# Kernel optimization log

Measured on AMD Instinct MI355X. Metric: run time of the kernel, lower is better.

Reference implementation:

```python
import jax, jax.numpy as jnp
import numpy as np

N_NODES = 100000
N_EDGES = 300000
HIDDEN = 256
N_TYPES = 8
VOCAB = 32000
N_STEPS = 5


def _gru_cell(x, h, w_ih, w_hh, b_ih, b_hh):
    # PyTorch GRUCell: gates ordered [reset, update, new]
    gi = x @ w_ih.T + b_ih                      # [N, 3H]
    gh = h @ w_hh.T + b_hh                      # [N, 3H]
    i_r, i_z, i_n = jnp.split(gi, 3, axis=-1)
    h_r, h_z, h_n = jnp.split(gh, 3, axis=-1)
    r = jax.nn.sigmoid(i_r + h_r)
    z = jax.nn.sigmoid(i_z + h_z)
    n = jnp.tanh(i_n + r * h_n)
    return (1.0 - z) * n + z * h


def _msg_op(h, edge_index, edge_type, W_msg, b_msg):
    # Gather source node states, apply per-edge-type linear, scatter-add to dst.
    src, dst = edge_index[0], edge_index[1]
    h_src = h[src]                               # [E, H]
    msgs = jnp.zeros_like(h_src)
    for t in range(N_TYPES):                     # small fixed loop over edge types
        m_t = h_src @ W_msg[t] + b_msg[t]        # [E, H]
        msgs = jnp.where((edge_type == t)[:, None], m_t, msgs)
    return jax.ops.segment_sum(msgs, dst, num_segments=h.shape[0])  # [N, H]


def setup_inputs() -> dict:
    key = jax.random.key(0)
    ks = jax.random.split(key, 10)
    x = jax.random.randint(ks[0], (N_NODES,), 0, VOCAB)
    edge_index = jax.random.randint(ks[1], (2, N_EDGES), 0, N_NODES)
    edge_type = jax.random.randint(ks[2], (N_EDGES,), 0, N_TYPES)
    s = 1.0 / np.sqrt(HIDDEN)
    emb = jax.random.normal(ks[3], (VOCAB, HIDDEN), dtype=jnp.float32)
    W_msg = jax.random.uniform(ks[4], (N_TYPES, HIDDEN, HIDDEN), minval=-s, maxval=s, dtype=jnp.float32)
    b_msg = jax.random.uniform(ks[5], (N_TYPES, HIDDEN), minval=-s, maxval=s, dtype=jnp.float32)
    w_ih = jax.random.uniform(ks[6], (3 * HIDDEN, HIDDEN), minval=-s, maxval=s, dtype=jnp.float32)
    w_hh = jax.random.uniform(ks[7], (3 * HIDDEN, HIDDEN), minval=-s, maxval=s, dtype=jnp.float32)
    b_ih = jax.random.uniform(ks[8], (3 * HIDDEN,), minval=-s, maxval=s, dtype=jnp.float32)
    b_hh = jax.random.uniform(ks[9], (3 * HIDDEN,), minval=-s, maxval=s, dtype=jnp.float32)
    return {"x": x, "edge_index": edge_index, "edge_type": edge_type,
            "emb": emb, "W_msg": W_msg, "b_msg": b_msg,
            "w_ih": w_ih, "w_hh": w_hh, "b_ih": b_ih, "b_hh": b_hh}


def reference(x, edge_index, edge_type, emb, W_msg, b_msg, w_ih, w_hh, b_ih, b_hh):
    h = emb[x]                                   # [N, H] node embedding lookup
    for _ in range(N_STEPS):
        aggr = _msg_op(h, edge_index, edge_type, W_msg, b_msg)
        h = _gru_cell(aggr, h, w_ih, w_hh, b_ih, b_hh)
    return h
```

## Files before the change

### kernel.cpp

```cpp
#include <hip/hip_runtime.h>
#include <math.h>

#define NN 100000
#define NE 300000
#define H 256
#define NT 8
#define NSTEPS 5
#define CHUNK 256
#define NB ((NE + CHUNK - 1) / CHUNK)
#define NBIN ((NN + 127) / 128)
#define MAXBIN 768
#define RS 264

typedef __attribute__((ext_vector_type(8))) short bf16x8;
typedef __attribute__((ext_vector_type(4))) float f32x4;

static __device__ __forceinline__ short f2bf(float f) {
    union { float f; unsigned u; } v; v.f = f;
    unsigned r = (v.u + 0x7FFFu + ((v.u >> 16) & 1u)) >> 16;
    return (short)r;
}
static __device__ __forceinline__ float bf2f(unsigned short s) {
    union { unsigned u; float f; } v; v.u = ((unsigned)s) << 16;
    return v.f;
}
static __device__ __forceinline__ float fexp2(float x) {
    float r; asm("v_exp_f32 %0, %1" : "=v"(r) : "v"(x)); return r;
}
static __device__ __forceinline__ float frcp(float x) {
    float r; asm("v_rcp_f32 %0, %1" : "=v"(r) : "v"(x)); return r;
}
#define LOG2E 1.442695041f

__global__ void k_embed(const int* __restrict__ x, const float* __restrict__ emb,
                        short* __restrict__ h) {
    int total = NN * 32;
    for (int idx = blockIdx.x * blockDim.x + threadIdx.x; idx < total;
         idx += gridDim.x * blockDim.x) {
        int node = idx >> 5;
        int c8 = (idx & 31) * 8;
        const float4* p = reinterpret_cast<const float4*>(
            emb + (size_t)x[node] * H + c8);
        float4 u0 = p[0], u1 = p[1];
        short t[8];
        t[0] = f2bf(u0.x); t[1] = f2bf(u0.y); t[2] = f2bf(u0.z); t[3] = f2bf(u0.w);
        t[4] = f2bf(u1.x); t[5] = f2bf(u1.y); t[6] = f2bf(u1.z); t[7] = f2bf(u1.w);
        *(bf16x8*)(h + (size_t)node * H + c8) = *(bf16x8*)t;
    }
}

__global__ void k_prep(const float* __restrict__ wih, const float* __restrict__ whh,
                       const float* __restrict__ Wm,
                       short* __restrict__ wihp, short* __restrict__ whhp,
                       short* __restrict__ Wmp) {
    const int NW = 3 * H * H;
    const int NM = NT * H * H;
    for (int i = blockIdx.x * blockDim.x + threadIdx.x; i < 2 * NW + NM;
         i += gridDim.x * blockDim.x) {
        if (i < 2 * NW) {
            int which = (i >= NW);
            int j = which ? i - NW : i;
            int m = j & 7, lane = (j >> 3) & 63;
            int cc = (j >> 9) & 15, kk = (j >> 13) & 7, gate = j >> 16;
            int row = gate * H + cc * 16 + (lane & 15);
            int col = kk * 32 + (lane >> 4) * 8 + m;
            const float* src = which ? whh : wih;
            (which ? whhp : wihp)[j] = f2bf(src[(size_t)row * H + col]);
        } else {
            int j = i - 2 * NW;
            int m = j & 7, lane = (j >> 3) & 63;
            int cc = (j >> 9) & 15, kk = (j >> 13) & 7, t = j >> 16;
            int jcol = cc * 16 + (lane & 15);
            int krow = kk * 32 + (lane >> 4) * 8 + m;
            Wmp[j] = f2bf(Wm[(size_t)t * H * H + (size_t)krow * H + jcol]);
        }
    }
}

__global__ void k_hist(const int* __restrict__ etype, int* __restrict__ hist_tb) {
    __shared__ int lh[NT];
    int b = blockIdx.x;
    if (threadIdx.x < NT) lh[threadIdx.x] = 0;
    __syncthreads();
    int e = b * CHUNK + threadIdx.x;
    if (e < NE) atomicAdd(&lh[etype[e]], 1);
    __syncthreads();
    if (threadIdx.x < NT) hist_tb[threadIdx.x * NB + b] = lh[threadIdx.x];
}

__global__ void k_scan(const int* __restrict__ hist_tb, int* __restrict__ off_tb,
                       int* __restrict__ pstart, int* __restrict__ perm) {
    __shared__ int total[NT];
    int t = threadIdx.x;
    if (t < NT) {
        int run = 0;
        for (int b = 0; b < NB; b++) {
            off_tb[t * NB + b] = run;
            run += hist_tb[t * NB + b];
        }
        total[t] = run;
    }
    __syncthreads();
    if (t == 0) {
        int p = 0;
        for (int tt = 0; tt < NT; tt++) {
            pstart[tt] = p;
            int padded = (total[tt] + 127) / 128 * 128;
            for (int q = total[tt]; q < padded; q++) perm[p + q] = -1;
            p += padded;
        }
        pstart[NT] = p;
    }
}

__global__ void k_scatter(const int* __restrict__ etype, const int* __restrict__ off_tb,
                          const int* __restrict__ pstart, int* __restrict__ perm) {
    __shared__ int st[CHUNK];
    int b = blockIdx.x;
    int e = b * CHUNK + threadIdx.x;
    st[threadIdx.x] = (e < NE) ? etype[e] : -1;
    __syncthreads();
    if (e < NE) {
        int t = st[threadIdx.x];
        int r = 0;
        for (int i = 0; i < threadIdx.x; i++) r += (st[i] == t);
        perm[pstart[t] + off_tb[t * NB + b] + r] = e;
    }
}

__global__ void k_hist2(const int* __restrict__ ei, int* __restrict__ hist2) {
    __shared__ int lh[NBIN];
    int b = blockIdx.x;
    for (int i = threadIdx.x; i < NBIN; i += 256) lh[i] = 0;
    __syncthreads();
    int e = b * CHUNK + threadIdx.x;
    if (e < NE) atomicAdd(&lh[ei[NE + e] >> 7], 1);
    __syncthreads();
    for (int i = threadIdx.x; i < NBIN; i += 256) hist2[i * NB + b] = lh[i];
}

__global__ void k_scan2a(const int* __restrict__ hist2, int* __restrict__ off2,
                         int* __restrict__ bintot) {
    int t = blockIdx.x * 256 + threadIdx.x;
    if (t >= NBIN) return;
    int run = 0;
    for (int c = 0; c < NB; c++) {
        off2[t * NB + c] = run;
        run += hist2[t * NB + c];
    }
    bintot[t] = run;
}

__global__ void k_scan2b(const int* __restrict__ bintot, int* __restrict__ binstart,
                         int* __restrict__ csr) {
    int p = 0;
    for (int b = 0; b < NBIN; b++) { binstart[b] = p; p += bintot[b]; }
    binstart[NBIN] = p;
    csr[NN] = NE;
}

__global__ void k_scatter2(const int* __restrict__ ei, const int* __restrict__ off2,
                           const int* __restrict__ binstart, int* __restrict__ ebin) {
    __shared__ short sb[CHUNK];
    int b = blockIdx.x;
    int e = b * CHUNK + threadIdx.x;
    int bin = (e < NE) ? (ei[NE + e] >> 7) : -1;
    sb[threadIdx.x] = (short)bin;
    __syncthreads();
    if (e < NE) {
        int r = 0;
        for (int i = 0; i < threadIdx.x; i++) r += (sb[i] == (short)bin);
        ebin[binstart[bin] + off2[bin * NB + b] + r] = e;
    }
}

__global__ __launch_bounds__(256) void k_lsort(
    const int* __restrict__ ei, const int* __restrict__ binstart,
    const int* __restrict__ ebin, int* __restrict__ csr, int* __restrict__ pos) {
    int b = blockIdx.x;
    int beg = binstart[b], cnt = binstart[b + 1] - beg;
    __shared__ unsigned short ld[MAXBIN];
    __shared__ int lh[128], ls[128];
    for (int i = threadIdx.x; i < 128; i += 256) lh[i] = 0;
    __syncthreads();
    for (int i = threadIdx.x; i < cnt; i += 256) {
        int d = ei[NE + ebin[beg + i]] & 127;
        ld[i] = (unsigned short)d;
        atomicAdd(&lh[d], 1);
    }
    __syncthreads();
    if (threadIdx.x == 0) {
        int run = 0;
        for (int l = 0; l < 128; l++) { ls[l] = run; run += lh[l]; }
    }
    __syncthreads();
    int base = b * 128;
    for (int l = threadIdx.x; l < 128; l += 256) {
        int dst = base + l;
        if (dst < NN) csr[dst] = beg + ls[l];
    }
    for (int i = threadIdx.x; i < cnt; i += 256) {
        int d = ld[i], r = 0;
        for (int j = 0; j < i; j++) r += (ld[j] == d);
        pos[ebin[beg + i]] = beg + ls[d] + r;
    }
}

__global__ __launch_bounds__(512) void k_msg(
    const int* __restrict__ perm, const int* __restrict__ pstart,
    const int* __restrict__ ei, const short* __restrict__ hcurb,
    const short* __restrict__ Wmp, const float* __restrict__ bm,
    const int* __restrict__ pos, short* __restrict__ msg) {
    int Epad = pstart[NT];
    int e0 = blockIdx.x * 128;
    if (e0 >= Epad) return;
    int t = 0;
    while (t < NT - 1 && e0 >= pstart[t + 1]) t++;

    __shared__ short sA[128][RS];
    __shared__ int se[128], pe[128];

    int tid = threadIdx.x;
    if (tid < 128) {
        int eid = perm[e0 + tid];
        se[tid] = (eid >= 0) ? ei[eid] : -1;
        pe[tid] = (eid >= 0) ? pos[eid] : -1;
    }
    __syncthreads();

    for (int task = tid; task < 1024; task += 512) {
        int r = task >> 3, c0 = (task & 7) * 32;
        int s = se[r];
        if (s >= 0) {
            const short* p = hcurb + (size_t)s * H + c0;
#pragma unroll
            for (int i = 0; i < 4; i++)
                *(bf16x8*)&sA[r][c0 + i * 8] = *(const bf16x8*)(p + i * 8);
        } else {
            bf16x8 z = {};
#pragma unroll
            for (int i = 0; i < 4; i++) *(bf16x8*)&sA[r][c0 + i * 8] = z;
        }
    }
    __syncthreads();

    int wid = tid >> 6, lane = tid & 63;
    int jw = wid * 32;
    int lr = lane & 15, lg = lane >> 4;

    f32x4 acc[8][2] = {};

    for (int kk = 0; kk < 8; kk++) {
        const short* fp = Wmp + (((size_t)(t * 8 + kk) * 16 + wid * 2) << 9) + lane * 8;
        bf16x8 fb[2];
        fb[0] = *(const bf16x8*)fp;
        fb[1] = *(const bf16x8*)(fp + 512);
        int k0 = kk * 32;
#pragma unroll
        for (int rh = 0; rh < 8; rh++) {
            bf16x8 fa = *(const bf16x8*)&sA[rh * 16 + lr][k0 + lg * 8];
#pragma unroll
            for (int ch = 0; ch < 2; ch++)
                acc[rh][ch] = __builtin_amdgcn_mfma_f32_16x16x32_bf16(
                    fa, fb[ch], acc[rh][ch], 0, 0, 0);
        }
    }

    __syncthreads();
    float bmv[2];
#pragma unroll
    for (int ch = 0; ch < 2; ch++) bmv[ch] = bm[t * H + jw + ch * 16 + lr];
#pragma unroll
    for (int rh = 0; rh < 8; rh++) {
#pragma unroll
        for (int reg = 0; reg < 4; reg++) {
            int row = rh * 16 + lg * 4 + reg;
#pragma unroll
            for (int ch = 0; ch < 2; ch++)
                sA[row][jw + ch * 16 + lr] = f2bf(acc[rh][ch][reg] + bmv[ch]);
        }
    }
    __syncthreads();
    for (int task = tid; task < 1024; task += 512) {
        int r = task >> 3, c0 = (task & 7) * 32;
        int p = pe[r];
        if (p < 0) continue;
        short* dstp = msg + (size_t)p * H + c0;
#pragma unroll
        for (int i = 0; i < 4; i++)
            *(bf16x8*)(dstp + i * 8) = *(bf16x8*)&sA[r][c0 + i * 8];
    }
}

__global__ __launch_bounds__(512)
__attribute__((amdgpu_waves_per_eu(2))) void k_gru(
    const short* __restrict__ msg, const int* __restrict__ csr,
    const short* __restrict__ hcurb, short* __restrict__ hnextb,
    float* __restrict__ outf,
    const short* __restrict__ wihp, const short* __restrict__ whhp,
    const float* __restrict__ bih, const float* __restrict__ bhh) {
    int n0 = blockIdx.x * 64;
    int tid = threadIdx.x;

    __shared__ short sA[64][RS];
    __shared__ short sH[64][RS];

    for (int task = tid; task < 1024; task += 512) {
        int which = task >> 9;
        int t2 = task & 511;
        int r = t2 >> 3, c0 = (t2 & 7) * 32;
        int n = n0 + r;
        if (which == 0) {
            float a[32];
#pragma unroll
            for (int i = 0; i < 32; i++) a[i] = 0.f;
            if (n < NN) {
                int beg = csr[n], end = csr[n + 1];
                for (int s = beg; s < end; s++) {
                    const short* mp = msg + (size_t)s * H + c0;
#pragma unroll
                    for (int i = 0; i < 4; i++) {
                        bf16x8 v = *(const bf16x8*)(mp + i * 8);
#pragma unroll
                        for (int m = 0; m < 8; m++)
                            a[i * 8 + m] += bf2f((unsigned short)v[m]);
                    }
                }
            }
            short tmp[32];
#pragma unroll
            for (int i = 0; i < 32; i++) tmp[i] = f2bf(a[i]);
#pragma unroll
            for (int i = 0; i < 4; i++)
                *(bf16x8*)&sA[r][c0 + i * 8] = *(bf16x8*)&tmp[i * 8];
        } else {
            if (n < NN) {
                const short* p = hcurb + (size_t)n * H + c0;
#pragma unroll
                for (int i = 0; i < 4; i++)
                    *(bf16x8*)&sH[r][c0 + i * 8] = *(const bf16x8*)(p + i * 8);
            } else {
                bf16x8 z = {};
#pragma unroll
                for (int i = 0; i < 4; i++) *(bf16x8*)&sH[r][c0 + i * 8] = z;
            }
        }
    }
    __syncthreads();

    int wid = tid >> 6, lane = tid & 63;
    int jw = wid * 32;
    int lr = lane & 15, lg = lane >> 4;

    f32x4 acc[4][4][2] = {};

    for (int kk = 0; kk < 8; kk++) {
        int k0 = kk * 32;
        bf16x8 fa[4], fh[4];
#pragma unroll
        for (int rh = 0; rh < 4; rh++) {
            fa[rh] = *(const bf16x8*)&sA[rh * 16 + lr][k0 + lg * 8];
            fh[rh] = *(const bf16x8*)&sH[rh * 16 + lr][k0 + lg * 8];
        }
#pragma unroll
        for (int g = 0; g < 6; g++) {
            const short* wp = (g & 1) ? whhp : wihp;
            int gate = g >> 1;
            int di = (g < 4) ? (g >> 1) : (g - 2);
            const short* fp = wp + (((size_t)(gate * 8 + kk) * 16 + wid * 2) << 9) + lane * 8;
            bf16x8 fb[2];
            fb[0] = *(const bf16x8*)fp;
            fb[1] = *(const bf16x8*)(fp + 512);
#pragma unroll
            for (int rh = 0; rh < 4; rh++)
#pragma unroll
                for (int ch = 0; ch < 2; ch++)
                    acc[di][rh][ch] = __builtin_amdgcn_mfma_f32_16x16x32_bf16(
                        (g & 1) ? fh[rh] : fa[rh], fb[ch], acc[di][rh][ch], 0, 0, 0);
        }
    }

    float b_r[2], b_z[2], b_in[2], b_hn[2];
#pragma unroll
    for (int ch = 0; ch < 2; ch++) {
        int jj = jw + ch * 16 + lr;
        b_r[ch]  = bih[jj] + bhh[jj];
        b_z[ch]  = bih[H + jj] + bhh[H + jj];
        b_in[ch] = bih[2 * H + jj];
        b_hn[ch] = bhh[2 * H + jj];
    }
#pragma unroll
    for (int rh = 0; rh < 4; rh++) {
#pragma unroll
        for (int reg = 0; reg < 4; reg++) {
            int row = rh * 16 + lg * 4 + reg;
            int n = n0 + row;
            if (n >= NN) continue;
#pragma unroll
            for (int ch = 0; ch < 2; ch++) {
                int jj = jw + ch * 16 + lr;
                float rr = acc[0][rh][ch][reg] + b_r[ch];
                float zz = acc[1][rh][ch][reg] + b_z[ch];
                float nn = acc[2][rh][ch][reg] + b_in[ch];
                float hn = acc[3][rh][ch][reg] + b_hn[ch];
                float r = frcp(1.f + fexp2(rr * -LOG2E));
                float z = frcp(1.f + fexp2(zz * -LOG2E));
                float x = nn + r * hn;
                float nv = 2.f * frcp(1.f + fexp2(x * -2.f * LOG2E)) - 1.f;
                float ho = bf2f((unsigned short)sH[row][jj]);
                float val = (1.f - z) * nv + z * ho;
                if (outf) outf[(size_t)n * H + jj] = val;
                else hnextb[(size_t)n * H + jj] = f2bf(val);
            }
        }
    }
}

extern "C" void kernel_launch(void* const* d_in, const int* in_sizes, int n_in,
                              void* d_out, int out_size, void* d_ws, size_t ws_size,
                              hipStream_t stream) {
    const int*   x     = (const int*)d_in[0];
    const int*   ei    = (const int*)d_in[1];
    const int*   etype = (const int*)d_in[2];
    const float* emb   = (const float*)d_in[3];
    const float* Wm    = (const float*)d_in[4];
    const float* bm    = (const float*)d_in[5];
    const float* wih   = (const float*)d_in[6];
    const float* whh   = (const float*)d_in[7];
    const float* bih   = (const float*)d_in[8];
    const float* bhh   = (const float*)d_in[9];

    float* out = (float*)d_out;

    short* hA    = (short*)d_ws;
    short* hB    = hA + (size_t)NN * H;
    short* wihp  = hB + (size_t)NN * H;
    short* whhp  = wihp + 3 * H * H;
    short* Wmp   = whhp + 3 * H * H;
    short* msg   = Wmp + NT * H * H;
    int* hist_tb = (int*)(msg + (size_t)NE * H);
    int* off_tb  = hist_tb + NT * NB;
    int* pstart  = off_tb + NT * NB;
    int* perm    = pstart + 16;
    int* hist2   = perm + NE + NT * 128;
    int* off2    = hist2 + NBIN * NB;
    int* bintot  = off2 + NBIN * NB;
    int* binstart= bintot + NBIN;
    int* ebin    = binstart + NBIN + 1;
    int* pos     = ebin + NE;
    int* csr     = pos + NE;

    k_embed<<<2048, 256, 0, stream>>>(x, emb, hA);
    k_prep<<<720, 256, 0, stream>>>(wih, whh, Wm, wihp, whhp, Wmp);

    k_hist<<<NB, CHUNK, 0, stream>>>(etype, hist_tb);
    k_scan<<<1, 64, 0, stream>>>(hist_tb, off_tb, pstart, perm);
    k_scatter<<<NB, CHUNK, 0, stream>>>(etype, off_tb, pstart, perm);

    k_hist2<<<NB, CHUNK, 0, stream>>>(ei, hist2);
    k_scan2a<<<(NBIN + 255) / 256, 256, 0, stream>>>(hist2, off2, bintot);
    k_scan2b<<<1, 1, 0, stream>>>(bintot, binstart, csr);
    k_scatter2<<<NB, CHUNK, 0, stream>>>(ei, off2, binstart, ebin);
    k_lsort<<<NBIN, 256, 0, stream>>>(ei, binstart, ebin, csr, pos);

    const int MSG_BX = (NE + NT * 128 + 127) / 128;
    const int GRU_BX = (NN + 63) / 64;

    short* hcur = hA;
    short* hnxt = hB;
    for (int s = 0; s < NSTEPS; s++) {
        int last = (s == NSTEPS - 1);
        k_msg<<<MSG_BX, 512, 0, stream>>>(perm, pstart, ei, hcur, Wmp, bm, pos, msg);
        k_gru<<<GRU_BX, 512, 0, stream>>>(msg, csr, hcur, hnxt,
                                          last ? out : nullptr,
                                          wihp, whhp, bih, bhh);
        short* tmp = hcur; hcur = hnxt; hnxt = tmp;
    }
}
```

Measured before the change: 1.635 ms.

## Halve msg tile to 64 edges, single-buffer GRU LDS, coalesce hidden-state stores

```diff
diff --git a/kernel.cpp b/kernel.cpp
--- a/kernel.cpp
+++ b/kernel.cpp
@@ -105,7 +105,7 @@
         int p = 0;
         for (int tt = 0; tt < NT; tt++) {
             pstart[tt] = p;
-            int padded = (total[tt] + 127) / 128 * 128;
+            int padded = (total[tt] + 63) / 64 * 64;
             for (int q = total[tt]; q < padded; q++) perm[p + q] = -1;
             p += padded;
         }
@@ -212,24 +212,24 @@
     const short* __restrict__ Wmp, const float* __restrict__ bm,
     const int* __restrict__ pos, short* __restrict__ msg) {
     int Epad = pstart[NT];
-    int e0 = blockIdx.x * 128;
+    int e0 = blockIdx.x * 64;
     if (e0 >= Epad) return;
     int t = 0;
     while (t < NT - 1 && e0 >= pstart[t + 1]) t++;
 
-    __shared__ short sA[128][RS];
-    __shared__ int se[128], pe[128];
+    __shared__ short sA[64][RS];
+    __shared__ int se[64], pe[64];
 
     int tid = threadIdx.x;
-    if (tid < 128) {
+    if (tid < 64) {
         int eid = perm[e0 + tid];
         se[tid] = (eid >= 0) ? ei[eid] : -1;
         pe[tid] = (eid >= 0) ? pos[eid] : -1;
     }
     __syncthreads();
 
-    for (int task = tid; task < 1024; task += 512) {
-        int r = task >> 3, c0 = (task & 7) * 32;
+    {
+        int r = tid >> 3, c0 = (tid & 7) * 32;
         int s = se[r];
         if (s >= 0) {
             const short* p = hcurb + (size_t)s * H + c0;
@@ -248,7 +248,7 @@
     int jw = wid * 32;
     int lr = lane & 15, lg = lane >> 4;
 
-    f32x4 acc[8][2] = {};
+    f32x4 acc[4][2] = {};
 
     for (int kk = 0; kk < 8; kk++) {
         const short* fp = Wmp + (((size_t)(t * 8 + kk) * 16 + wid * 2) << 9) + lane * 8;
@@ -257,7 +257,7 @@
         fb[1] = *(const bf16x8*)(fp + 512);
         int k0 = kk * 32;
 #pragma unroll
-        for (int rh = 0; rh < 8; rh++) {
+        for (int rh = 0; rh < 4; rh++) {
             bf16x8 fa = *(const bf16x8*)&sA[rh * 16 + lr][k0 + lg * 8];
 #pragma unroll
             for (int ch = 0; ch < 2; ch++)
@@ -271,7 +271,7 @@
 #pragma unroll
     for (int ch = 0; ch < 2; ch++) bmv[ch] = bm[t * H + jw + ch * 16 + lr];
 #pragma unroll
-    for (int rh = 0; rh < 8; rh++) {
+    for (int rh = 0; rh < 4; rh++) {
 #pragma unroll
         for (int reg = 0; reg < 4; reg++) {
             int row = rh * 16 + lg * 4 + reg;
@@ -281,14 +281,15 @@
         }
     }
     __syncthreads();
-    for (int task = tid; task < 1024; task += 512) {
-        int r = task >> 3, c0 = (task & 7) * 32;
+    {
+        int r = tid >> 3, c0 = (tid & 7) * 32;
         int p = pe[r];
-        if (p < 0) continue;
-        short* dstp = msg + (size_t)p * H + c0;
-#pragma unroll
-        for (int i = 0; i < 4; i++)
-            *(bf16x8*)(dstp + i * 8) = *(bf16x8*)&sA[r][c0 + i * 8];
+        if (p >= 0) {
+            short* dstp = msg + (size_t)p * H + c0;
+#pragma unroll
+            for (int i = 0; i < 4; i++)
+                *(bf16x8*)(dstp + i * 8) = *(bf16x8*)&sA[r][c0 + i * 8];
+        }
     }
 }
 
@@ -302,72 +303,52 @@
     int n0 = blockIdx.x * 64;
     int tid = threadIdx.x;
 
-    __shared__ short sA[64][RS];
-    __shared__ short sH[64][RS];
-
-    for (int task = tid; task < 1024; task += 512) {
-        int which = task >> 9;
-        int t2 = task & 511;
-        int r = t2 >> 3, c0 = (t2 & 7) * 32;
-        int n = n0 + r;
-        if (which == 0) {
-            float a[32];
-#pragma unroll
-            for (int i = 0; i < 32; i++) a[i] = 0.f;
-            if (n < NN) {
-                int beg = csr[n], end = csr[n + 1];
-                for (int s = beg; s < end; s++) {
-                    const short* mp = msg + (size_t)s * H + c0;
-#pragma unroll
-                    for (int i = 0; i < 4; i++) {
-                        bf16x8 v = *(const bf16x8*)(mp + i * 8);
-#pragma unroll
-                        for (int m = 0; m < 8; m++)
-                            a[i * 8 + m] += bf2f((unsigned short)v[m]);
-                    }
-                }
-            }
-            short tmp[32];
-#pragma unroll
-            for (int i = 0; i < 32; i++) tmp[i] = f2bf(a[i]);
-#pragma unroll
-            for (int i = 0; i < 4; i++)
-                *(bf16x8*)&sA[r][c0 + i * 8] = *(bf16x8*)&tmp[i * 8];
-        } else {
-            if (n < NN) {
-                const short* p = hcurb + (size_t)n * H + c0;
-#pragma unroll
-                for (int i = 0; i < 4; i++)
-                    *(bf16x8*)&sH[r][c0 + i * 8] = *(const bf16x8*)(p + i * 8);
-            } else {
-                bf16x8 z = {};
-#pragma unroll
-                for (int i = 0; i < 4; i++) *(bf16x8*)&sH[r][c0 + i * 8] = z;
-            }
-        }
-    }
-    __syncthreads();
+    __shared__ short sX[64][RS];
 
     int wid = tid >> 6, lane = tid & 63;
     int jw = wid * 32;
     int lr = lane & 15, lg = lane >> 4;
 
+    {
+        int r = tid >> 3, c0 = (tid & 7) * 32;
+        int n = n0 + r;
+        float a[32];
+#pragma unroll
+        for (int i = 0; i < 32; i++) a[i] = 0.f;
+        if (n < NN) {
+            int beg = csr[n], end = csr[n + 1];
+            for (int s = beg; s < end; s++) {
+                const short* mp = msg + (size_t)s * H + c0;
+#pragma unroll
+                for (int i = 0; i < 4; i++) {
+                    bf16x8 v = *(const bf16x8*)(mp + i * 8);
+#pragma unroll
+                    for (int m = 0; m < 8; m++)
+                        a[i * 8 + m] += bf2f((unsigned short)v[m]);
+                }
+            }
+        }
+        short tmp[32];
+#pragma unroll
+        for (int i = 0; i < 32; i++) tmp[i] = f2bf(a[i]);
+#pragma unroll
+        for (int i = 0; i < 4; i++)
+            *(bf16x8*)&sX[r][c0 + i * 8] = *(bf16x8*)&tmp[i * 8];
+    }
+    __syncthreads();
+
     f32x4 acc[4][4][2] = {};
 
     for (int kk = 0; kk < 8; kk++) {
         int k0 = kk * 32;
-        bf16x8 fa[4], fh[4];
-#pragma unroll
-        for (int rh = 0; rh < 4; rh++) {
-            fa[rh] = *(const bf16x8*)&sA[rh * 16 + lr][k0 + lg * 8];
-            fh[rh] = *(const bf16x8*)&sH[rh * 16 + lr][k0 + lg * 8];
-        }
-#pragma unroll
-        for (int g = 0; g < 6; g++) {
-            const short* wp = (g & 1) ? whhp : wihp;
-            int gate = g >> 1;
-            int di = (g < 4) ? (g >> 1) : (g - 2);
-            const short* fp = wp + (((size_t)(gate * 8 + kk) * 16 + wid * 2) << 9) + lane * 8;
+        bf16x8 fa[4];
+#pragma unroll
+        for (int rh = 0; rh < 4; rh++)
+            fa[rh] = *(const bf16x8*)&sX[rh * 16 + lr][k0 + lg * 8];
+#pragma unroll
+        for (int gate = 0; gate < 3; gate++) {
+            int di = (gate < 2) ? gate : 2;
+            const short* fp = wihp + (((size_t)(gate * 8 + kk) * 16 + wid * 2) << 9) + lane * 8;
             bf16x8 fb[2];
             fb[0] = *(const bf16x8*)fp;
             fb[1] = *(const bf16x8*)(fp + 512);
@@ -376,7 +357,46 @@
 #pragma unroll
                 for (int ch = 0; ch < 2; ch++)
                     acc[di][rh][ch] = __builtin_amdgcn_mfma_f32_16x16x32_bf16(
-                        (g & 1) ? fh[rh] : fa[rh], fb[ch], acc[di][rh][ch], 0, 0, 0);
+                        fa[rh], fb[ch], acc[di][rh][ch], 0, 0, 0);
+        }
+    }
+    __syncthreads();
+
+    {
+        int r = tid >> 3, c0 = (tid & 7) * 32;
+        int n = n0 + r;
+        if (n < NN) {
+            const short* p = hcurb + (size_t)n * H + c0;
+#pragma unroll
+            for (int i = 0; i < 4; i++)
+                *(bf16x8*)&sX[r][c0 + i * 8] = *(const bf16x8*)(p + i * 8);
+        } else {
+            bf16x8 z = {};
+#pragma unroll
+            for (int i = 0; i < 4; i++) *(bf16x8*)&sX[r][c0 + i * 8] = z;
+        }
+    }
+    __syncthreads();
+
+    for (int kk = 0; kk < 8; kk++) {
+        int k0 = kk * 32;
+        bf16x8 fh[4];
+#pragma unroll
+        for (int rh = 0; rh < 4; rh++)
+            fh[rh] = *(const bf16x8*)&sX[rh * 16 + lr][k0 + lg * 8];
+#pragma unroll
+        for (int gate = 0; gate < 3; gate++) {
+            int di = (gate < 2) ? gate : 3;
+            const short* fp = whhp + (((size_t)(gate * 8 + kk) * 16 + wid * 2) << 9) + lane * 8;
+            bf16x8 fb[2];
+            fb[0] = *(const bf16x8*)fp;
+            fb[1] = *(const bf16x8*)(fp + 512);
+#pragma unroll
+            for (int rh = 0; rh < 4; rh++)
+#pragma unroll
+                for (int ch = 0; ch < 2; ch++)
+                    acc[di][rh][ch] = __builtin_amdgcn_mfma_f32_16x16x32_bf16(
+                        fh[rh], fb[ch], acc[di][rh][ch], 0, 0, 0);
         }
     }
 
@@ -389,13 +409,12 @@
         b_in[ch] = bih[2 * H + jj];
         b_hn[ch] = bhh[2 * H + jj];
     }
+    float vals[32];
 #pragma unroll
     for (int rh = 0; rh < 4; rh++) {
 #pragma unroll
         for (int reg = 0; reg < 4; reg++) {
             int row = rh * 16 + lg * 4 + reg;
-            int n = n0 + row;
-            if (n >= NN) continue;
 #pragma unroll
             for (int ch = 0; ch < 2; ch++) {
                 int jj = jw + ch * 16 + lr;
@@ -407,11 +426,43 @@
                 float z = frcp(1.f + fexp2(zz * -LOG2E));
                 float x = nn + r * hn;
                 float nv = 2.f * frcp(1.f + fexp2(x * -2.f * LOG2E)) - 1.f;
-                float ho = bf2f((unsigned short)sH[row][jj]);
-                float val = (1.f - z) * nv + z * ho;
-                if (outf) outf[(size_t)n * H + jj] = val;
-                else hnextb[(size_t)n * H + jj] = f2bf(val);
+                float ho = bf2f((unsigned short)sX[row][jj]);
+                vals[(rh * 4 + reg) * 2 + ch] = (1.f - z) * nv + z * ho;
             }
+        }
+    }
+    if (outf) {
+#pragma unroll
+        for (int rh = 0; rh < 4; rh++)
+#pragma unroll
+            for (int reg = 0; reg < 4; reg++) {
+                int n = n0 + rh * 16 + lg * 4 + reg;
+                if (n >= NN) continue;
+#pragma unroll
+                for (int ch = 0; ch < 2; ch++)
+                    outf[(size_t)n * H + jw + ch * 16 + lr] =
+                        vals[(rh * 4 + reg) * 2 + ch];
+            }
+    } else {
+        __syncthreads();
+#pragma unroll
+        for (int rh = 0; rh < 4; rh++)
+#pragma unroll
+            for (int reg = 0; reg < 4; reg++) {
+                int row = rh * 16 + lg * 4 + reg;
+#pragma unroll
+                for (int ch = 0; ch < 2; ch++)
+                    sX[row][jw + ch * 16 + lr] =
+                        f2bf(vals[(rh * 4 + reg) * 2 + ch]);
+            }
+        __syncthreads();
+        int r = tid >> 3, c0 = (tid & 7) * 32;
+        int n = n0 + r;
+        if (n < NN) {
+            short* dstp = hnextb + (size_t)n * H + c0;
+#pragma unroll
+            for (int i = 0; i < 4; i++)
+                *(bf16x8*)(dstp + i * 8) = *(bf16x8*)&sX[r][c0 + i * 8];
         }
     }
 }
@@ -442,7 +493,7 @@
     int* off_tb  = hist_tb + NT * NB;
     int* pstart  = off_tb + NT * NB;
     int* perm    = pstart + 16;
-    int* hist2   = perm + NE + NT * 128;
+    int* hist2   = perm + NE + NT * 64;
     int* off2    = hist2 + NBIN * NB;
     int* bintot  = off2 + NBIN * NB;
     int* binstart= bintot + NBIN;
@@ -463,7 +514,7 @@
     k_scatter2<<<NB, CHUNK, 0, stream>>>(ei, off2, binstart, ebin);
     k_lsort<<<NBIN, 256, 0, stream>>>(ei, binstart, ebin, csr, pos);
 
-    const int MSG_BX = (NE + NT * 128 + 127) / 128;
+    const int MSG_BX = (NE + NT * 64 + 63) / 64;
     const int GRU_BX = (NN + 63) / 64;
 
     short* hcur = hA;
```

After: 1.810 ms. +10.7%, slower.
